# Optimization experiments

Measured on AMD Instinct MI355X. Metric: run time of the kernel, lower is better.

The kernel has to match this reference:

```python
import jax, jax.numpy as jnp
import numpy as np


def setup_inputs() -> dict:
    key = jax.random.key(0)
    images = jax.random.uniform(key, (64, 384, 384, 3), dtype=jnp.float32)
    return {"images": images, "k": 5}


def reference(images, k):
    # cv2.dilate with a k x k kernel of ones == per-channel max filter with SAME padding.
    # Applied over the whole batch in one fused reduce_window (window only over H, W).
    out = jax.lax.reduce_window(
        images,
        -jnp.inf,
        jax.lax.max,
        window_dimensions=(1, k, k, 1),
        window_strides=(1, 1, 1, 1),
        padding="SAME",
    )
    # cv_to_tf appends a trailing singleton dim before tf.stack -> (B, H, W, C, 1)
    return out[..., None]
```

## Files before the change

kernel.cpp:

```cpp
#include <hip/hip_runtime.h>
#include <hip/hip_bf16.h>


#define Bn 64
#define H 384
#define ROWF 1152
#define ROWBYTES (ROWF * 4)
#define WF4 288
#define RB 16
#define GROUPS 6
#define STRIPS 5
#define NEGINF (-3.402823466e+38f)

__device__ __forceinline__ float4 max4(float4 a, float4 b) {
  return make_float4(fmaxf(a.x, b.x), fmaxf(a.y, b.y),
                     fmaxf(a.z, b.z), fmaxf(a.w, b.w));
}

struct Batch { float4 A, B, C, D, E; };

__global__ __launch_bounds__(256) void dilate5_kernel(
    const float* __restrict__ in, float* __restrict__ out) {
  const int wv = threadIdx.x >> 6;
  const int lane = threadIdx.x & 63;
  int t = blockIdx.x;
  const int strip = t % STRIPS; t /= STRIPS;
  const int grp = t % GROUPS;   t /= GROUPS;
  const int b = t;

  const int row0 = (grp * 4 + wv) * RB;
  const int c = strip * 64 + lane;
  const bool active = (c < WF4);
  const int cc = active ? c : (WF4 - 1);

  const int cA = (cc - 2 >= 0) ? cc - 2 : 0;
  const int cB = (cc - 1 >= 0) ? cc - 1 : 0;
  const int cD = (cc + 1 < WF4) ? cc + 1 : WF4 - 1;
  const int cE = (cc + 2 < WF4) ? cc + 2 : WF4 - 1;
  const int offA = cA * 16, offB = cB * 16, offC = cc * 16,
            offD = cD * 16, offE = cE * 16;
  const bool mA = (c >= 2), mB = (c >= 1), mD = (c + 1 < WF4), mE = (c + 2 < WF4);
  const float4 ninf = make_float4(NEGINF, NEGINF, NEGINF, NEGINF);

  const char* __restrict__ imgb = (const char*)in + (size_t)b * H * ROWBYTES;
  char* __restrict__ outb = (char*)out + (size_t)b * H * ROWBYTES;

  auto loadrow = [&](int gh) -> Batch {
    int ghc = gh < 0 ? 0 : (gh > H - 1 ? H - 1 : gh);
    const char* rb = imgb + (size_t)ghc * ROWBYTES;
    Batch L;
    L.A = *reinterpret_cast<const float4*>(rb + offA);
    L.B = *reinterpret_cast<const float4*>(rb + offB);
    L.C = *reinterpret_cast<const float4*>(rb + offC);
    L.D = *reinterpret_cast<const float4*>(rb + offD);
    L.E = *reinterpret_cast<const float4*>(rb + offE);
    return L;
  };

  auto hcomb = [&](int gh, const Batch& L) -> float4 {
    float4 A  = mA ? L.A : ninf;
    float4 Bv = mB ? L.B : ninf;
    float4 Cv = L.C;
    float4 D  = mD ? L.D : ninf;
    float4 E  = mE ? L.E : ninf;
    float4 h;
    h.x = fmaxf(fmaxf(fmaxf(A.z, Bv.y), fmaxf(Cv.x, Cv.w)), D.z);
    h.y = fmaxf(fmaxf(fmaxf(A.w, Bv.z), fmaxf(Cv.y, D.x)), D.w);
    h.z = fmaxf(fmaxf(fmaxf(Bv.x, Bv.w), fmaxf(Cv.z, D.y)), E.x);
    h.w = fmaxf(fmaxf(fmaxf(Bv.y, Cv.x), fmaxf(Cv.w, D.z)), E.y);
    if (gh < 0 || gh >= H) h = ninf;
    return h;
  };

  float4 r0 = hcomb(row0 - 2, loadrow(row0 - 2));
  float4 r1 = hcomb(row0 - 1, loadrow(row0 - 1));
  float4 r2 = hcomb(row0,     loadrow(row0));
  float4 r3 = hcomb(row0 + 1, loadrow(row0 + 1));
  Batch Lc = loadrow(row0 + 2);

#pragma unroll 4
  for (int i = 0; i < RB; ++i) {
    const int o = row0 + i;
    Batch Ln = loadrow(o + 3);
    float4 r4 = hcomb(o + 2, Lc);
    float4 v = max4(max4(max4(r0, r1), max4(r2, r3)), r4);
    if (active)
      *reinterpret_cast<float4*>(outb + (size_t)o * ROWBYTES + offC) = v;
    r0 = r1; r1 = r2; r2 = r3; r3 = r4;
    Lc = Ln;
  }
}

extern "C" void kernel_launch(void* const* d_in, const int* in_sizes, int n_in,
                              void* d_out, int out_size, void* d_ws, size_t ws_size,
                              hipStream_t stream) {
  const float* images = (const float*)d_in[0];
  float* out = (float*)d_out;
  const int nblocks = Bn * GROUPS * STRIPS;
  dilate5_kernel<<<nblocks, 256, 0, stream>>>(images, out);
}
```

Measured before the change: 212.1 us.

## Replace five neighbor loads with one load plus wavefront shuffles for halo

Each lane now loads only its own float4 per row, and neighbors obtain the left/right float4s through __shfl_up/__shfl_down across the 64-lane wavefront. Strips now overlap by two columns on each side, so each wave computes 60 output columns and the edge lanes act as halo only. This cuts global load instructions per row from five to one and deepens prefetch to two rows ahead. In exchange it adds cross-lane shuffle instructions and slightly redundant halo loads. The grid stays at 5 strips, which still covers the 288 float4 columns.

```diff
diff --git a/kernel.cpp b/kernel.cpp
--- a/kernel.cpp
+++ b/kernel.cpp
@@ -10,14 +10,21 @@
 #define RB 16
 #define GROUPS 6
 #define STRIPS 5
+#define SOUT 60
 #define NEGINF (-3.402823466e+38f)
 
 __device__ __forceinline__ float4 max4(float4 a, float4 b) {
   return make_float4(fmaxf(a.x, b.x), fmaxf(a.y, b.y),
                      fmaxf(a.z, b.z), fmaxf(a.w, b.w));
 }
-
-struct Batch { float4 A, B, C, D, E; };
+__device__ __forceinline__ float4 shflup4(float4 v, int d) {
+  return make_float4(__shfl_up(v.x, d), __shfl_up(v.y, d),
+                     __shfl_up(v.z, d), __shfl_up(v.w, d));
+}
+__device__ __forceinline__ float4 shfldn4(float4 v, int d) {
+  return make_float4(__shfl_down(v.x, d), __shfl_down(v.y, d),
+                     __shfl_down(v.z, d), __shfl_down(v.w, d));
+}
 
 __global__ __launch_bounds__(256) void dilate5_kernel(
     const float* __restrict__ in, float* __restrict__ out) {
@@ -29,40 +36,27 @@
   const int b = t;
 
   const int row0 = (grp * 4 + wv) * RB;
-  const int c = strip * 64 + lane;
-  const bool active = (c < WF4);
-  const int cc = active ? c : (WF4 - 1);
+  const int col = strip * SOUT - 2 + lane;
+  const bool cvalid = (col >= 0) && (col < WF4);
+  const int ccl = col < 0 ? 0 : (col > WF4 - 1 ? WF4 - 1 : col);
+  const size_t coff = (size_t)ccl * 16;
+  const bool willstore = (lane >= 2) && (lane < 62) && (col < WF4);
 
-  const int cA = (cc - 2 >= 0) ? cc - 2 : 0;
-  const int cB = (cc - 1 >= 0) ? cc - 1 : 0;
-  const int cD = (cc + 1 < WF4) ? cc + 1 : WF4 - 1;
-  const int cE = (cc + 2 < WF4) ? cc + 2 : WF4 - 1;
-  const int offA = cA * 16, offB = cB * 16, offC = cc * 16,
-            offD = cD * 16, offE = cE * 16;
-  const bool mA = (c >= 2), mB = (c >= 1), mD = (c + 1 < WF4), mE = (c + 2 < WF4);
   const float4 ninf = make_float4(NEGINF, NEGINF, NEGINF, NEGINF);
-
   const char* __restrict__ imgb = (const char*)in + (size_t)b * H * ROWBYTES;
   char* __restrict__ outb = (char*)out + (size_t)b * H * ROWBYTES;
 
-  auto loadrow = [&](int gh) -> Batch {
+  auto loadC = [&](int gh) -> float4 {
     int ghc = gh < 0 ? 0 : (gh > H - 1 ? H - 1 : gh);
-    const char* rb = imgb + (size_t)ghc * ROWBYTES;
-    Batch L;
-    L.A = *reinterpret_cast<const float4*>(rb + offA);
-    L.B = *reinterpret_cast<const float4*>(rb + offB);
-    L.C = *reinterpret_cast<const float4*>(rb + offC);
-    L.D = *reinterpret_cast<const float4*>(rb + offD);
-    L.E = *reinterpret_cast<const float4*>(rb + offE);
-    return L;
+    float4 v = *reinterpret_cast<const float4*>(imgb + (size_t)ghc * ROWBYTES + coff);
+    return cvalid ? v : ninf;
   };
 
-  auto hcomb = [&](int gh, const Batch& L) -> float4 {
-    float4 A  = mA ? L.A : ninf;
-    float4 Bv = mB ? L.B : ninf;
-    float4 Cv = L.C;
-    float4 D  = mD ? L.D : ninf;
-    float4 E  = mE ? L.E : ninf;
+  auto hcomb = [&](int gh, float4 Cv) -> float4 {
+    float4 A = shflup4(Cv, 2);
+    float4 Bv = shflup4(Cv, 1);
+    float4 D = shfldn4(Cv, 1);
+    float4 E = shfldn4(Cv, 2);
     float4 h;
     h.x = fmaxf(fmaxf(fmaxf(A.z, Bv.y), fmaxf(Cv.x, Cv.w)), D.z);
     h.y = fmaxf(fmaxf(fmaxf(A.w, Bv.z), fmaxf(Cv.y, D.x)), D.w);
@@ -72,22 +66,27 @@
     return h;
   };
 
-  float4 r0 = hcomb(row0 - 2, loadrow(row0 - 2));
-  float4 r1 = hcomb(row0 - 1, loadrow(row0 - 1));
-  float4 r2 = hcomb(row0,     loadrow(row0));
-  float4 r3 = hcomb(row0 + 1, loadrow(row0 + 1));
-  Batch Lc = loadrow(row0 + 2);
+  float4 C0 = loadC(row0 - 2);
+  float4 C1 = loadC(row0 - 1);
+  float4 C2 = loadC(row0);
+  float4 C3 = loadC(row0 + 1);
+  float4 Cc = loadC(row0 + 2);
+  float4 Cn = loadC(row0 + 3);
+  float4 r0 = hcomb(row0 - 2, C0);
+  float4 r1 = hcomb(row0 - 1, C1);
+  float4 r2 = hcomb(row0,     C2);
+  float4 r3 = hcomb(row0 + 1, C3);
 
 #pragma unroll 4
   for (int i = 0; i < RB; ++i) {
     const int o = row0 + i;
-    Batch Ln = loadrow(o + 3);
-    float4 r4 = hcomb(o + 2, Lc);
+    float4 Cf = loadC(o + 4);
+    float4 r4 = hcomb(o + 2, Cc);
     float4 v = max4(max4(max4(r0, r1), max4(r2, r3)), r4);
-    if (active)
-      *reinterpret_cast<float4*>(outb + (size_t)o * ROWBYTES + offC) = v;
+    if (willstore)
+      *reinterpret_cast<float4*>(outb + (size_t)o * ROWBYTES + coff) = v;
     r0 = r1; r1 = r2; r2 = r3; r3 = r4;
-    Lc = Ln;
+    Cc = Cn; Cn = Cf;
   }
 }
 
```

Measured after the change: 214.0 us. No clear change (+0.9%).
